# Kernel tuning notes

Measured on AMD Instinct MI355X. Metric: run time of the kernel, lower is better.

The kernel has to match this reference:

```python
import jax, jax.numpy as jnp
import numpy as np

EPS = 1e-10  # matches torch float32 path


def setup_inputs() -> dict:
    key = jax.random.key(0)
    ks = jax.random.split(key, 8)
    B, E, D, N = 32, 32000, 128, 1000
    scale = 1.0 / np.sqrt(D)
    return {
        "edge_attr": jax.random.normal(ks[0], (B, E, D), dtype=jnp.float32),
        "edge_index": jax.random.randint(ks[1], (B, 2, E), 0, N, dtype=jnp.int64),
        "W1": jax.random.normal(ks[2], (D, D), dtype=jnp.float32) * scale,
        "b1": jax.random.normal(ks[3], (D,), dtype=jnp.float32) * 0.01,
        "W2": jax.random.normal(ks[4], (D, D), dtype=jnp.float32) * scale,
        "b2": jax.random.normal(ks[5], (D,), dtype=jnp.float32) * 0.01,
        "Wout": jax.random.normal(ks[6], (1, D), dtype=jnp.float32) * scale,
        "bout": jax.random.normal(ks[7], (1,), dtype=jnp.float32) * 0.01,
        "num_nodes": N,
    }


def reference(edge_attr, edge_index, W1, b1, W2, b2, Wout, bout, num_nodes):
    # Edge MLP: (num_layers-1)=2 hidden silu linears, then 1-dim sigmoid output
    x = jax.nn.silu(jnp.einsum("bed,fd->bef", edge_attr, W1) + b1)
    x = jax.nn.silu(jnp.einsum("bed,fd->bef", x, W2) + b2)
    vals = jax.nn.sigmoid(jnp.einsum("bed,od->beo", x, Wout) + bout)[..., 0]  # [B, E]
    B = vals.shape[0]
    b_idx = jnp.arange(B)[:, None]  # [B, 1] broadcasts over E
    heatmap = jnp.zeros((B, num_nodes, num_nodes), dtype=vals.dtype)
    heatmap = heatmap.at[b_idx, edge_index[:, 0], edge_index[:, 1]].set(vals)
    return jnp.log(heatmap + EPS)
```

## Files before the change

### kernel.cpp

```cpp
#include <hip/hip_runtime.h>
#include <stdint.h>
#include <string.h>
#include <math.h>

typedef __bf16 bf16x8 __attribute__((ext_vector_type(8)));
typedef float f32x4 __attribute__((ext_vector_type(4)));
typedef unsigned short us8 __attribute__((ext_vector_type(8)));
typedef unsigned int u32;

#define DD 128

__device__ __forceinline__ unsigned short f2bf(float f) {
    __bf16 b = (__bf16)f;
    return __builtin_bit_cast(unsigned short, b);
}
__device__ __forceinline__ u32 pack2(float a, float b) {
    return (u32)f2bf(a) | ((u32)f2bf(b) << 16);
}
__device__ __forceinline__ float fsilu(float x) {
    float e = __expf(-x);
    return x * __builtin_amdgcn_rcpf(1.0f + e);
}

__global__ void fill_const(u32* __restrict__ p, long n4, u32 val) {
    long i  = (long)blockIdx.x * blockDim.x + threadIdx.x;
    long st = (long)gridDim.x * blockDim.x;
    uint4 v4 = make_uint4(val, val, val, val);
    for (long k = i; k < n4; k += st) ((uint4*)p)[k] = v4;
}

__device__ __forceinline__ float decz(u32 u) {
    float z = (float)(int)(u & 0x3FFFu) * (1.0f / 256.0f) - 40.0f;
    float s = __builtin_amdgcn_rcpf(1.0f + __expf(-z));
    return __logf(s + 1e-10f);
}
__global__ void decode_sparse(u32* __restrict__ p, long n4) {
    long i  = (long)blockIdx.x * blockDim.x + threadIdx.x;
    long st = (long)gridDim.x * blockDim.x;
    for (long k = i; k < n4; k += st) {
        uint4 u = ((const uint4*)p)[k];
        float* f = (float*)(p + k * 4);
        if (u.x >= 0xE0000000u) f[0] = decz(u.x);
        if (u.y >= 0xE0000000u) f[1] = decz(u.y);
        if (u.z >= 0xE0000000u) f[2] = decz(u.z);
        if (u.w >= 0xE0000000u) f[3] = decz(u.w);
    }
}

__global__ __launch_bounds__(1024)
void mlp_scatter(const float* __restrict__ A,
                 const int* __restrict__ eidx,
                 const float* __restrict__ W1, const float* __restrict__ B1,
                 const float* __restrict__ W2, const float* __restrict__ B2,
                 const float* __restrict__ WO, const float* __restrict__ BO,
                 u32* __restrict__ out,
                 int E, int nWT, int N)
{
    extern __shared__ char smem[];
    unsigned short* W1s = (unsigned short*)smem;
    unsigned short* W2s = (unsigned short*)(smem + 32768);
    float* b1s = (float*)(smem + 65536);
    float* b2s = (float*)(smem + 66048);
    float* wos = (float*)(smem + 66560);
    char*  Hs  = smem + 67072;

    const int tid  = threadIdx.x;
    const int lane = tid & 63;
    const int wave = tid >> 6;
    const int lrow = lane & 15;
    const int lg   = lane >> 4;

    #pragma unroll
    for (int c = 0; c < 2; ++c) {
        int id = c * 1024 + tid;
        int f  = id >> 4;
        int kb = (id & 15) * 8;
        const float* s1 = W1 + f * DD + kb;
        const float* s2 = W2 + f * DD + kb;
        float4 a0 = *(const float4*)s1, a1 = *(const float4*)(s1 + 4);
        float4 c0 = *(const float4*)s2, c1 = *(const float4*)(s2 + 4);
        us8 t1, t2;
        t1[0]=f2bf(a0.x); t1[1]=f2bf(a0.y); t1[2]=f2bf(a0.z); t1[3]=f2bf(a0.w);
        t1[4]=f2bf(a1.x); t1[5]=f2bf(a1.y); t1[6]=f2bf(a1.z); t1[7]=f2bf(a1.w);
        t2[0]=f2bf(c0.x); t2[1]=f2bf(c0.y); t2[2]=f2bf(c0.z); t2[3]=f2bf(c0.w);
        t2[4]=f2bf(c1.x); t2[5]=f2bf(c1.y); t2[6]=f2bf(c1.z); t2[7]=f2bf(c1.w);
        int off = f * 256 + ((kb * 2) ^ ((f & 7) << 4));
        *(us8*)((char*)W1s + off) = t1;
        *(us8*)((char*)W2s + off) = t2;
    }
    if (tid < DD) { b1s[tid] = B1[tid]; b2s[tid] = B2[tid]; wos[tid] = WO[tid]; }
    const float bo = BO[0];
    const size_t NN = (size_t)N * (size_t)N;
    char* HsW = Hs + wave * 4096;
    __syncthreads();

    const int wid  = blockIdx.x * 16 + wave;
    const int step = (int)gridDim.x * 16;

    for (int wt = wid; wt < nWT; wt += step) {
        const int r0  = wt << 4;
        const int b   = r0 / E;
        const int ei0 = r0 - b * E;
        int i0 = 0, j0 = 0;
        if (lane < 16) {
            i0 = eidx[(size_t)(2 * b) * E + ei0 + lane];
            j0 = eidx[(size_t)(2 * b + 1) * E + ei0 + lane];
        }

        const float* Ar = A + (size_t)(r0 + lrow) * DD;
        float4 e0[4], e1[4];
        #pragma unroll
        for (int kk = 0; kk < 4; ++kk) {
            const float* p = Ar + kk * 32 + lg * 8;
            e0[kk] = *(const float4*)p;
            e1[kk] = *(const float4*)(p + 4);
        }

        f32x4 acc[8];
        #pragma unroll
        for (int mt = 0; mt < 8; ++mt)
            acc[mt] = *(const f32x4*)&b1s[mt * 16 + lg * 4];
        #pragma unroll
        for (int kk = 0; kk < 4; ++kk) {
            us8 t;
            t[0]=f2bf(e0[kk].x); t[1]=f2bf(e0[kk].y); t[2]=f2bf(e0[kk].z); t[3]=f2bf(e0[kk].w);
            t[4]=f2bf(e1[kk].x); t[5]=f2bf(e1[kk].y); t[6]=f2bf(e1[kk].z); t[7]=f2bf(e1[kk].w);
            bf16x8 ef = __builtin_bit_cast(bf16x8, t);
            #pragma unroll
            for (int mt = 0; mt < 8; ++mt) {
                int f = mt * 16 + lrow;
                bf16x8 wf = *(const bf16x8*)((const char*)W1s + f * 256 +
                                             ((kk * 64 + lg * 16) ^ ((f & 7) << 4)));
                acc[mt] = __builtin_amdgcn_mfma_f32_16x16x32_bf16(wf, ef, acc[mt], 0, 0, 0);
            }
        }

        #pragma unroll
        for (int mt = 0; mt < 8; ++mt) {
            u32 p0 = pack2(fsilu(acc[mt][0]), fsilu(acc[mt][1]));
            u32 p1 = pack2(fsilu(acc[mt][2]), fsilu(acc[mt][3]));
            *(uint2*)(HsW + lrow * 256 + ((mt * 32 + lg * 8) ^ ((lrow & 7) << 4))) =
                make_uint2(p0, p1);
        }

        f32x4 acc2[8];
        #pragma unroll
        for (int mt = 0; mt < 8; ++mt)
            acc2[mt] = *(const f32x4*)&b2s[mt * 16 + lg * 4];
        #pragma unroll
        for (int kk = 0; kk < 4; ++kk) {
            bf16x8 hf = *(const bf16x8*)(HsW + lrow * 256 +
                                         ((kk * 64 + lg * 16) ^ ((lrow & 7) << 4)));
            #pragma unroll
            for (int mt = 0; mt < 8; ++mt) {
                int f = mt * 16 + lrow;
                bf16x8 wf = *(const bf16x8*)((const char*)W2s + f * 256 +
                                             ((kk * 64 + lg * 16) ^ ((f & 7) << 4)));
                acc2[mt] = __builtin_amdgcn_mfma_f32_16x16x32_bf16(wf, hf, acc2[mt], 0, 0, 0);
            }
        }

        float zp = 0.f;
        #pragma unroll
        for (int mt = 0; mt < 8; ++mt) {
            f32x4 w4 = *(const f32x4*)&wos[mt * 16 + lg * 4];
            zp += w4[0] * fsilu(acc2[mt][0]) + w4[1] * fsilu(acc2[mt][1])
                + w4[2] * fsilu(acc2[mt][2]) + w4[3] * fsilu(acc2[mt][3]);
        }
        zp += __shfl_xor(zp, 16);
        zp += __shfl_xor(zp, 32);

        if (lane < 16) {
            float z = zp + bo;
            int qz = (int)((z + 40.0f) * 256.0f + 0.5f);
            qz = qz < 0 ? 0 : (qz > 16383 ? 16383 : qz);
            u32 packed = 0xE0000000u | ((u32)(ei0 + lane + 1) << 14) | (u32)qz;
            atomicMax(&out[(size_t)b * NN + (size_t)i0 * N + (size_t)j0], packed);
        }
    }
}

extern "C" void kernel_launch(void* const* d_in, const int* in_sizes, int n_in,
                              void* d_out, int out_size, void* d_ws, size_t ws_size,
                              hipStream_t stream) {
    const float* edge_attr  = (const float*)d_in[0];
    const int*   edge_index = (const int*)d_in[1];
    const float* W1   = (const float*)d_in[2];
    const float* b1   = (const float*)d_in[3];
    const float* W2   = (const float*)d_in[4];
    const float* b2   = (const float*)d_in[5];
    const float* Wout = (const float*)d_in[6];
    const float* bout = (const float*)d_in[7];

    long rows = (long)in_sizes[0] / DD;
    int  E    = in_sizes[1] / 64;
    int  nWT  = (int)(rows / 16);
    int  Bb   = (int)(rows / E);
    int  N    = (int)(sqrtf((float)(out_size / Bb)) + 0.5f);

    u32* outp = (u32*)d_out;
    long n4 = (long)out_size >> 2;

    float fv = logf(1e-10f);
    u32 FB; memcpy(&FB, &fv, 4);

    const int SMEM = 132608;
    hipFuncSetAttribute((const void*)mlp_scatter,
                        hipFuncAttributeMaxDynamicSharedMemorySize, SMEM);

    fill_const<<<2048, 256, 0, stream>>>(outp, n4, FB);
    mlp_scatter<<<256, 1024, SMEM, stream>>>(edge_attr, edge_index, W1, b1, W2, b2,
                                             Wout, bout, outp, E, nWT, N);
    decode_sparse<<<2048, 256, 0, stream>>>(outp, n4);
}
```

Measured before the change: 217.5 us.

## Switch MLP to FP8 MFMA with 32-edge wave tiles and smaller blocks

Replaces the bf16 MFMA path with fp8 (16x16x32 fp8) MFMAs. Weights are pre-packed into an MFMA-fragment-ordered shared layout instead of swizzled bf16 rows. Each wave now processes 32 edges (two N tiles) so every weight fragment load feeds two MFMAs. Blocks shrink to 256 threads with static shared memory and a grid of 1536, which allows more blocks per CU. FP8 quantization of inputs, weights and hidden activations lowers accuracy and may break the tolerance; the 32-edge tiling also assumes E is divisible by 32.

```diff
diff --git a/kernel.cpp b/kernel.cpp
--- a/kernel.cpp
+++ b/kernel.cpp
@@ -3,23 +3,19 @@
 #include <string.h>
 #include <math.h>
 
-typedef __bf16 bf16x8 __attribute__((ext_vector_type(8)));
 typedef float f32x4 __attribute__((ext_vector_type(4)));
-typedef unsigned short us8 __attribute__((ext_vector_type(8)));
 typedef unsigned int u32;
 
 #define DD 128
-
-__device__ __forceinline__ unsigned short f2bf(float f) {
-    __bf16 b = (__bf16)f;
-    return __builtin_bit_cast(unsigned short, b);
-}
-__device__ __forceinline__ u32 pack2(float a, float b) {
-    return (u32)f2bf(a) | ((u32)f2bf(b) << 16);
-}
+#define NE 32
+
 __device__ __forceinline__ float fsilu(float x) {
     float e = __expf(-x);
     return x * __builtin_amdgcn_rcpf(1.0f + e);
+}
+__device__ __forceinline__ u32 pk4fp8(float a, float b, float c, float d) {
+    u32 r = __builtin_amdgcn_cvt_pk_fp8_f32(a, b, 0u, false);
+    return __builtin_amdgcn_cvt_pk_fp8_f32(c, d, r, true);
 }
 
 __global__ void fill_const(u32* __restrict__ p, long n4, u32 val) {
@@ -47,22 +43,19 @@
     }
 }
 
-__global__ __launch_bounds__(1024)
+__global__ __launch_bounds__(256)
 void mlp_scatter(const float* __restrict__ A,
                  const int* __restrict__ eidx,
                  const float* __restrict__ W1, const float* __restrict__ B1,
                  const float* __restrict__ W2, const float* __restrict__ B2,
                  const float* __restrict__ WO, const float* __restrict__ BO,
                  u32* __restrict__ out,
-                 int E, int nWT, int N)
+                 int E, int nWT, int tpw, int N)
 {
-    extern __shared__ char smem[];
-    unsigned short* W1s = (unsigned short*)smem;
-    unsigned short* W2s = (unsigned short*)(smem + 32768);
-    float* b1s = (float*)(smem + 65536);
-    float* b2s = (float*)(smem + 66048);
-    float* wos = (float*)(smem + 66560);
-    char*  Hs  = smem + 67072;
+    __shared__ uint2 W1s[8][4][64];
+    __shared__ uint2 W2s[8][4][64];
+    __shared__ float b1s[DD], b2s[DD], wos[DD];
+    __shared__ uint2 Hs[4][2][4][64];
 
     const int tid  = threadIdx.x;
     const int lane = tid & 63;
@@ -71,107 +64,115 @@
     const int lg   = lane >> 4;
 
     #pragma unroll
-    for (int c = 0; c < 2; ++c) {
-        int id = c * 1024 + tid;
-        int f  = id >> 4;
-        int kb = (id & 15) * 8;
-        const float* s1 = W1 + f * DD + kb;
-        const float* s2 = W2 + f * DD + kb;
-        float4 a0 = *(const float4*)s1, a1 = *(const float4*)(s1 + 4);
-        float4 c0 = *(const float4*)s2, c1 = *(const float4*)(s2 + 4);
-        us8 t1, t2;
-        t1[0]=f2bf(a0.x); t1[1]=f2bf(a0.y); t1[2]=f2bf(a0.z); t1[3]=f2bf(a0.w);
-        t1[4]=f2bf(a1.x); t1[5]=f2bf(a1.y); t1[6]=f2bf(a1.z); t1[7]=f2bf(a1.w);
-        t2[0]=f2bf(c0.x); t2[1]=f2bf(c0.y); t2[2]=f2bf(c0.z); t2[3]=f2bf(c0.w);
-        t2[4]=f2bf(c1.x); t2[5]=f2bf(c1.y); t2[6]=f2bf(c1.z); t2[7]=f2bf(c1.w);
-        int off = f * 256 + ((kb * 2) ^ ((f & 7) << 4));
-        *(us8*)((char*)W1s + off) = t1;
-        *(us8*)((char*)W2s + off) = t2;
+    for (int c = 0; c < 8; ++c) {
+        int id = c * 256 + tid;
+        int mt = id >> 8, kk = (id >> 6) & 3, ln = id & 63;
+        const float* p1 = W1 + (mt * 16 + (ln & 15)) * DD + kk * 32 + (ln >> 4) * 8;
+        const float* p2 = W2 + (mt * 16 + (ln & 15)) * DD + kk * 32 + (ln >> 4) * 8;
+        float4 x0 = *(const float4*)p1, x1 = *(const float4*)(p1 + 4);
+        float4 y0 = *(const float4*)p2, y1 = *(const float4*)(p2 + 4);
+        W1s[mt][kk][ln] = make_uint2(pk4fp8(x0.x, x0.y, x0.z, x0.w),
+                                     pk4fp8(x1.x, x1.y, x1.z, x1.w));
+        W2s[mt][kk][ln] = make_uint2(pk4fp8(y0.x, y0.y, y0.z, y0.w),
+                                     pk4fp8(y1.x, y1.y, y1.z, y1.w));
     }
     if (tid < DD) { b1s[tid] = B1[tid]; b2s[tid] = B2[tid]; wos[tid] = WO[tid]; }
     const float bo = BO[0];
     const size_t NN = (size_t)N * (size_t)N;
-    char* HsW = Hs + wave * 4096;
     __syncthreads();
 
-    const int wid  = blockIdx.x * 16 + wave;
-    const int step = (int)gridDim.x * 16;
+    const int wid  = blockIdx.x * 4 + wave;
+    const int step = (int)gridDim.x * 4;
 
     for (int wt = wid; wt < nWT; wt += step) {
-        const int r0  = wt << 4;
-        const int b   = r0 / E;
-        const int ei0 = r0 - b * E;
+        const int b   = wt / tpw;
+        const int ei0 = (wt - b * tpw) * NE;
+        const long r0 = (long)wt * NE;
+
         int i0 = 0, j0 = 0;
-        if (lane < 16) {
+        if (lane < NE) {
             i0 = eidx[(size_t)(2 * b) * E + ei0 + lane];
             j0 = eidx[(size_t)(2 * b + 1) * E + ei0 + lane];
         }
 
-        const float* Ar = A + (size_t)(r0 + lrow) * DD;
-        float4 e0[4], e1[4];
+        float4 va[2][4][2];
+        #pragma unroll
+        for (int nt = 0; nt < 2; ++nt)
+            #pragma unroll
+            for (int kk = 0; kk < 4; ++kk) {
+                const float* p = A + (r0 + nt * 16 + lrow) * DD + kk * 32 + lg * 8;
+                va[nt][kk][0] = *(const float4*)p;
+                va[nt][kk][1] = *(const float4*)(p + 4);
+            }
+        uint2 ef[2][4];
+        #pragma unroll
+        for (int nt = 0; nt < 2; ++nt)
+            #pragma unroll
+            for (int kk = 0; kk < 4; ++kk)
+                ef[nt][kk] = make_uint2(
+                    pk4fp8(va[nt][kk][0].x, va[nt][kk][0].y, va[nt][kk][0].z, va[nt][kk][0].w),
+                    pk4fp8(va[nt][kk][1].x, va[nt][kk][1].y, va[nt][kk][1].z, va[nt][kk][1].w));
+
+        f32x4 acc[8][2];
+        #pragma unroll
+        for (int mt = 0; mt < 8; ++mt) {
+            f32x4 bi = *(const f32x4*)&b1s[mt * 16 + lg * 4];
+            acc[mt][0] = bi; acc[mt][1] = bi;
+        }
+        #pragma unroll
+        for (int kk = 0; kk < 4; ++kk)
+            #pragma unroll
+            for (int mt = 0; mt < 8; ++mt) {
+                long wf = __builtin_bit_cast(long, W1s[mt][kk][lane]);
+                #pragma unroll
+                for (int nt = 0; nt < 2; ++nt)
+                    acc[mt][nt] = __builtin_amdgcn_mfma_f32_16x16x32_fp8_fp8(
+                        wf, __builtin_bit_cast(long, ef[nt][kk]), acc[mt][nt], 0, 0, 0);
+            }
+
+        #pragma unroll
+        for (int mt = 0; mt < 8; ++mt) {
+            int lnp = (((mt & 1) << 1) | (lg >> 1)) * 16 + lrow;
+            #pragma unroll
+            for (int nt = 0; nt < 2; ++nt) {
+                u32 pw = pk4fp8(fsilu(acc[mt][nt][0]), fsilu(acc[mt][nt][1]),
+                                fsilu(acc[mt][nt][2]), fsilu(acc[mt][nt][3]));
+                ((u32*)&Hs[wave][nt][mt >> 1][lnp])[lg & 1] = pw;
+            }
+        }
+
+        f32x4 acc2[8][2];
+        #pragma unroll
+        for (int mt = 0; mt < 8; ++mt) {
+            f32x4 bi = *(const f32x4*)&b2s[mt * 16 + lg * 4];
+            acc2[mt][0] = bi; acc2[mt][1] = bi;
+        }
         #pragma unroll
         for (int kk = 0; kk < 4; ++kk) {
-            const float* p = Ar + kk * 32 + lg * 8;
-            e0[kk] = *(const float4*)p;
-            e1[kk] = *(const float4*)(p + 4);
-        }
-
-        f32x4 acc[8];
-        #pragma unroll
-        for (int mt = 0; mt < 8; ++mt)
-            acc[mt] = *(const f32x4*)&b1s[mt * 16 + lg * 4];
-        #pragma unroll
-        for (int kk = 0; kk < 4; ++kk) {
-            us8 t;
-            t[0]=f2bf(e0[kk].x); t[1]=f2bf(e0[kk].y); t[2]=f2bf(e0[kk].z); t[3]=f2bf(e0[kk].w);
-            t[4]=f2bf(e1[kk].x); t[5]=f2bf(e1[kk].y); t[6]=f2bf(e1[kk].z); t[7]=f2bf(e1[kk].w);
-            bf16x8 ef = __builtin_bit_cast(bf16x8, t);
+            long hf0 = __builtin_bit_cast(long, Hs[wave][0][kk][lane]);
+            long hf1 = __builtin_bit_cast(long, Hs[wave][1][kk][lane]);
             #pragma unroll
             for (int mt = 0; mt < 8; ++mt) {
-                int f = mt * 16 + lrow;
-                bf16x8 wf = *(const bf16x8*)((const char*)W1s + f * 256 +
-                                             ((kk * 64 + lg * 16) ^ ((f & 7) << 4)));
-                acc[mt] = __builtin_amdgcn_mfma_f32_16x16x32_bf16(wf, ef, acc[mt], 0, 0, 0);
-            }
-        }
-
-        #pragma unroll
-        for (int mt = 0; mt < 8; ++mt) {
-            u32 p0 = pack2(fsilu(acc[mt][0]), fsilu(acc[mt][1]));
-            u32 p1 = pack2(fsilu(acc[mt][2]), fsilu(acc[mt][3]));
-            *(uint2*)(HsW + lrow * 256 + ((mt * 32 + lg * 8) ^ ((lrow & 7) << 4))) =
-                make_uint2(p0, p1);
-        }
-
-        f32x4 acc2[8];
-        #pragma unroll
-        for (int mt = 0; mt < 8; ++mt)
-            acc2[mt] = *(const f32x4*)&b2s[mt * 16 + lg * 4];
-        #pragma unroll
-        for (int kk = 0; kk < 4; ++kk) {
-            bf16x8 hf = *(const bf16x8*)(HsW + lrow * 256 +
-                                         ((kk * 64 + lg * 16) ^ ((lrow & 7) << 4)));
-            #pragma unroll
-            for (int mt = 0; mt < 8; ++mt) {
-                int f = mt * 16 + lrow;
-                bf16x8 wf = *(const bf16x8*)((const char*)W2s + f * 256 +
-                                             ((kk * 64 + lg * 16) ^ ((f & 7) << 4)));
-                acc2[mt] = __builtin_amdgcn_mfma_f32_16x16x32_bf16(wf, hf, acc2[mt], 0, 0, 0);
-            }
-        }
-
-        float zp = 0.f;
+                long wf = __builtin_bit_cast(long, W2s[mt][kk][lane]);
+                acc2[mt][0] = __builtin_amdgcn_mfma_f32_16x16x32_fp8_fp8(wf, hf0, acc2[mt][0], 0, 0, 0);
+                acc2[mt][1] = __builtin_amdgcn_mfma_f32_16x16x32_fp8_fp8(wf, hf1, acc2[mt][1], 0, 0, 0);
+            }
+        }
+
+        float zp0 = 0.f, zp1 = 0.f;
         #pragma unroll
         for (int mt = 0; mt < 8; ++mt) {
             f32x4 w4 = *(const f32x4*)&wos[mt * 16 + lg * 4];
-            zp += w4[0] * fsilu(acc2[mt][0]) + w4[1] * fsilu(acc2[mt][1])
-                + w4[2] * fsilu(acc2[mt][2]) + w4[3] * fsilu(acc2[mt][3]);
-        }
-        zp += __shfl_xor(zp, 16);
-        zp += __shfl_xor(zp, 32);
-
-        if (lane < 16) {
-            float z = zp + bo;
+            zp0 += w4[0] * fsilu(acc2[mt][0][0]) + w4[1] * fsilu(acc2[mt][0][1])
+                 + w4[2] * fsilu(acc2[mt][0][2]) + w4[3] * fsilu(acc2[mt][0][3]);
+            zp1 += w4[0] * fsilu(acc2[mt][1][0]) + w4[1] * fsilu(acc2[mt][1][1])
+                 + w4[2] * fsilu(acc2[mt][1][2]) + w4[3] * fsilu(acc2[mt][1][3]);
+        }
+        zp0 += __shfl_xor(zp0, 16); zp0 += __shfl_xor(zp0, 32);
+        zp1 += __shfl_xor(zp1, 16); zp1 += __shfl_xor(zp1, 32);
+
+        if (lane < NE) {
+            float z = ((lane >> 4) ? zp1 : zp0) + bo;
             int qz = (int)((z + 40.0f) * 256.0f + 0.5f);
             qz = qz < 0 ? 0 : (qz > 16383 ? 16383 : qz);
             u32 packed = 0xE0000000u | ((u32)(ei0 + lane + 1) << 14) | (u32)qz;
@@ -194,7 +195,8 @@
 
     long rows = (long)in_sizes[0] / DD;
     int  E    = in_sizes[1] / 64;
-    int  nWT  = (int)(rows / 16);
+    int  nWT  = (int)(rows / NE);
+    int  tpw  = E / NE;
     int  Bb   = (int)(rows / E);
     int  N    = (int)(sqrtf((float)(out_size / Bb)) + 0.5f);
 
@@ -204,12 +206,8 @@
     float fv = logf(1e-10f);
     u32 FB; memcpy(&FB, &fv, 4);
 
-    const int SMEM = 132608;
-    hipFuncSetAttribute((const void*)mlp_scatter,
-                        hipFuncAttributeMaxDynamicSharedMemorySize, SMEM);
-
     fill_const<<<2048, 256, 0, stream>>>(outp, n4, FB);
-    mlp_scatter<<<256, 1024, SMEM, stream>>>(edge_attr, edge_index, W1, b1, W2, b2,
-                                             Wout, bout, outp, E, nWT, N);
+    mlp_scatter<<<1536, 256, 0, stream>>>(edge_attr, edge_index, W1, b1, W2, b2,
+                                          Wout, bout, outp, E, nWT, tpw, N);
     decode_sparse<<<2048, 256, 0, stream>>>(outp, n4);
 }
```

New measurement: 285.0 us. 31.0% more time.
